# Kernel optimization log

Hardware: AMD Instinct MI355X
Metric: run time of the kernel (lower is better)

Reference implementation:

```python
import jax, jax.numpy as jnp
import numpy as np

# ---- static forest structure: 1024 complete binary trees of depth 9 ----
N_TREES = 1024
DEPTH = 9
NPT = 2 ** (DEPTH + 1) - 1            # 1023 nodes per tree
DIM = N_TREES * NPT                    # 1,047,552 total nodes
C = 10                                 # hidden states
M = 128                                # emission alphabet
N_GEN = 4                              # parallel generative models
LEVEL_SIZES = [N_TREES * 2 ** (k + 1) for k in range(DEPTH)]
LEVEL_START = np.concatenate([[0], np.cumsum(LEVEL_SIZES)]).astype(np.int64)
TREE_OFF = np.arange(N_TREES, dtype=np.int64) * NPT


def _build_forest():
    parents, children = [], []
    for k in range(DEPTH):
        ch = np.arange(2 ** (k + 1) - 1, 2 ** (k + 2) - 1, dtype=np.int64)  # depth k+1 nodes
        pa = (ch - 1) // 2                                                   # their parents (depth k)
        children.append((TREE_OFF[:, None] + ch[None, :]).ravel())
        parents.append((TREE_OFF[:, None] + pa[None, :]).ravel())
    leaves = (TREE_OFF[:, None] + np.arange(NPT // 2, NPT, dtype=np.int64)[None, :]).ravel()
    trees_ind = np.repeat(np.arange(N_TREES, dtype=np.int64), NPT)
    return np.concatenate(parents), np.concatenate(children), leaves, trees_ind


def setup_inputs() -> dict:
    key = jax.random.key(0)
    k1, k2, k3, k4 = jax.random.split(key, 4)
    parents, children, leaves, trees_ind = _build_forest()
    return {
        "x": jax.random.randint(k4, (DIM,), 0, M, dtype=jnp.int32),
        "A": jax.random.normal(k1, (C, C, N_GEN), jnp.float32) * 2.5,
        "B": jax.random.normal(k2, (C, M, N_GEN), jnp.float32) * 2.5,
        "Pi": jax.random.normal(k3, (C, N_GEN), jnp.float32) * 2.5,
        "parents": jnp.asarray(parents, jnp.int32),
        "children": jnp.asarray(children, jnp.int32),
        "trees_ind": jnp.asarray(trees_ind, jnp.int32),
        "leaves": jnp.asarray(leaves, jnp.int32),
    }


def _upward(x, A, B, Pi, parents, children, trees_ind, leaves):
    # softmax reparameterization (vectorized over the n_gen axis)
    smA = jax.nn.softmax(A, axis=0)    # P(parent state i | child state j), cols sum over i
    smB = jax.nn.softmax(B, axis=1)    # emission distribution per state
    smPi = jax.nn.softmax(Pi, axis=0)  # leaf prior

    beta = jnp.zeros((DIM, C, N_GEN), smA.dtype)
    t_beta = jnp.zeros((DIM, C, N_GEN), smA.dtype)
    ll = jnp.zeros((DIM, N_GEN), smA.dtype)

    # leaves: beta = Pi * B[:, x_leaf], normalized
    B_leaf = jnp.swapaxes(smB[:, x[leaves]], 0, 1)            # [L, C, G]
    b = smPi[None, :, :] * B_leaf
    nu = b.sum(axis=1)                                         # [L, G]
    beta = beta.at[leaves].set(b / nu[:, None, :])
    ll = ll.at[leaves].set(jnp.log(nu))

    # bottom-up sweep over levels (static loop over tree depth)
    for k in reversed(range(DEPTH)):
        s, e = int(LEVEL_START[k]), int(LEVEL_START[k + 1])
        pa, ch = parents[s:e], children[s:e]
        beta_ch = beta[ch]                                     # [E, C, G]
        tb_ch = jnp.einsum('ijg,ejg->eig', smA, beta_ch)       # sum over child state j
        sums = jax.ops.segment_sum(tb_ch, pa, num_segments=DIM)
        cnt = jax.ops.segment_sum(jnp.ones((e - s,), smA.dtype), pa, num_segments=DIM)
        t_beta = t_beta + sums / jnp.maximum(cnt, 1.0)[:, None, None]  # scatter-mean over children
        # unique parents at this level = all depth-k nodes (static for complete trees)
        u = jnp.asarray((TREE_OFF[:, None] + np.arange(2 ** k - 1, 2 ** (k + 1) - 1)[None, :]).ravel(), jnp.int32)
        B_u = jnp.swapaxes(smB[:, x[u]], 0, 1)                 # [U, C, G]
        bl = t_beta[u] * B_u
        nu = bl.sum(axis=1)
        beta = beta.at[u].set(bl / nu[:, None, :])
        ll = ll.at[u].set(jnp.log(nu))

    # per-tree log-likelihood: scatter-sum node terms over trees_ind
    return jax.ops.segment_sum(ll, trees_ind, num_segments=N_TREES)  # [n_trees, G]


def reference(x, A, B, Pi, parents, children, trees_ind, leaves):
    return _upward(x, A, B, Pi, parents, children, trees_ind, leaves)
```

## Files before the change

kernel.cpp:

```cpp
#include <hip/hip_runtime.h>
#include <math.h>

#define NC     10
#define NCP    12
#define NM     128
#define NGEN   4
#define NPT    1023
#define NTREES 1024

#define RCPF(x) __builtin_amdgcn_rcpf(x)
#define WAVE_FENCE() __builtin_amdgcn_wave_barrier()

struct F12 { float4 a, b, c; };

__device__ __forceinline__ F12 ld12(const float* p) {
    F12 r; const float4* q = (const float4*)p;
    r.a = q[0]; r.b = q[1]; r.c = q[2]; return r;
}
__device__ __forceinline__ void unpack10(float* t, const F12& r) {
    t[0] = r.a.x; t[1] = r.a.y; t[2] = r.a.z; t[3] = r.a.w;
    t[4] = r.b.x; t[5] = r.b.y; t[6] = r.b.z; t[7] = r.b.w;
    t[8] = r.c.x; t[9] = r.c.y;
}
__device__ __forceinline__ void fma10(float* t, const F12& c, float s) {
    t[0] += c.a.x * s; t[1] += c.a.y * s; t[2] += c.a.z * s; t[3] += c.a.w * s;
    t[4] += c.b.x * s; t[5] += c.b.y * s; t[6] += c.b.z * s; t[7] += c.b.w * s;
    t[8] += c.c.x * s; t[9] += c.c.y * s;
}
__device__ __forceinline__ void mul10(float* t, const F12& r) {
    t[0] *= r.a.x; t[1] *= r.a.y; t[2] *= r.a.z; t[3] *= r.a.w;
    t[4] *= r.b.x; t[5] *= r.b.y; t[6] *= r.b.z; t[7] *= r.b.w;
    t[8] *= r.c.x; t[9] *= r.c.y;
}
__device__ __forceinline__ float sum10(const float* v) {
    return (((v[0] + v[1]) + (v[2] + v[3])) + ((v[4] + v[5]) + (v[6] + v[7]))) + (v[8] + v[9]);
}

__device__ __forceinline__ float half_subtree(const F12* acol,
                                              const float (*sBT)[NCP],
                                              const float (*sBTpi)[NCP],
                                              int xl0, int xl1, int xl2, int xl3,
                                              int x8a, int x8b, int x7, float* b7out)
{
    float b0[NC], b1[NC], sc[NC], t8a[NC], t8b[NC];

    unpack10(b0, ld12(&sBTpi[xl0][0]));
    unpack10(b1, ld12(&sBTpi[xl1][0]));
    float nu0 = sum10(b0), nu1 = sum10(b1);
    #pragma unroll
    for (int j = 0; j < NC; ++j) sc[j] = b0[j] * nu1 + b1[j] * nu0;
    #pragma unroll
    for (int i = 0; i < NC; ++i) t8a[i] = 0.f;
    #pragma unroll
    for (int j = 0; j < NC; ++j) fma10(t8a, acol[j], sc[j]);
    mul10(t8a, ld12(&sBT[x8a][0]));
    const float nu8a = sum10(t8a);

    unpack10(b0, ld12(&sBTpi[xl2][0]));
    unpack10(b1, ld12(&sBTpi[xl3][0]));
    nu0 = sum10(b0); nu1 = sum10(b1);
    #pragma unroll
    for (int j = 0; j < NC; ++j) sc[j] = b0[j] * nu1 + b1[j] * nu0;
    #pragma unroll
    for (int i = 0; i < NC; ++i) t8b[i] = 0.f;
    #pragma unroll
    for (int j = 0; j < NC; ++j) fma10(t8b, acol[j], sc[j]);
    mul10(t8b, ld12(&sBT[x8b][0]));
    const float nu8b = sum10(t8b);

    #pragma unroll
    for (int j = 0; j < NC; ++j) sc[j] = t8a[j] * nu8b + t8b[j] * nu8a;
    float t7[NC];
    #pragma unroll
    for (int i = 0; i < NC; ++i) t7[i] = 0.f;
    #pragma unroll
    for (int j = 0; j < NC; ++j) fma10(t7, acol[j], sc[j]);
    mul10(t7, ld12(&sBT[x7][0]));
    const float nu7 = sum10(t7);
    const float r = RCPF(nu7);
    #pragma unroll
    for (int j = 0; j < NC; ++j) b7out[j] = t7[j] * r;
    return __logf(nu7);
}

__device__ __forceinline__ float fused_step_ip(const F12* acol, const float (*sBT)[NCP],
                                               float* buf, int l,
                                               int xc0, int xc1, int xp)
{
    float t0[NC], t1[NC];
    #pragma unroll
    for (int i = 0; i < NC; ++i) { t0[i] = 0.f; t1[i] = 0.f; }
    #pragma unroll
    for (int j = 0; j < NC; ++j) {
        float4 gv = *(const float4*)(buf + j * 64 + 4 * l);
        fma10(t0, acol[j], gv.x + gv.y);
        fma10(t1, acol[j], gv.z + gv.w);
    }
    mul10(t0, ld12(&sBT[xc0][0]));
    mul10(t1, ld12(&sBT[xc1][0]));
    const float nu0 = sum10(t0), nu1 = sum10(t1);
    float tp[NC];
    #pragma unroll
    for (int i = 0; i < NC; ++i) tp[i] = 0.f;
    #pragma unroll
    for (int j = 0; j < NC; ++j) fma10(tp, acol[j], t0[j] * nu1 + t1[j] * nu0);
    mul10(tp, ld12(&sBT[xp][0]));
    const float nup = sum10(tp);
    const float rp = RCPF(nup);
    #pragma unroll
    for (int j = 0; j < NC; ++j) buf[j * 64 + l] = tp[j] * rp;
    return __logf(nup);
}

__global__ __launch_bounds__(256, 2)
void htmm_fused(const int* __restrict__ x,
                const float* __restrict__ A,
                const float* __restrict__ B,
                const float* __restrict__ Pi,
                float* __restrict__ out)
{
    __shared__ __align__(16) float sACol[NC][NCP];
    __shared__ __align__(16) float sBT[NM][NCP];
    __shared__ __align__(16) float sBTpi[NM][NCP];
    __shared__ __align__(16) float sPiP[NCP];
    __shared__ __align__(16) float sB6[4][NC][64];

    const int bid = blockIdx.x;
    const int g = bid >> 8;
    const int treeBase = (bid & 255) * 4;
    const int tid = threadIdx.x;
    const int u = tid >> 6, lane = tid & 63;

    const int tree = treeBase + u;
    const int tb = tree * NPT;

    int xl[8];
    #pragma unroll
    for (int k = 0; k < 8; ++k) xl[k] = x[tb + 511 + 8 * lane + k];
    int x8v[4];
    #pragma unroll
    for (int c = 0; c < 4; ++c) x8v[c] = x[tb + 255 + 4 * lane + c];
    const int x7a = x[tb + 127 + 2 * lane];
    const int x7b = x[tb + 128 + 2 * lane];
    const int x6v = x[tb + 63 + lane];

    for (int c = u; c < NC; c += 4) {
        float e0 = __expf(B[(c * NM + lane) * NGEN + g]);
        float e1 = __expf(B[(c * NM + lane + 64) * NGEN + g]);
        float sm = e0 + e1;
        #pragma unroll
        for (int off = 32; off; off >>= 1) sm += __shfl_xor(sm, off);
        const float rs = 1.f / sm;
        sBT[lane][c]      = e0 * rs;
        sBT[lane + 64][c] = e1 * rs;
    }
    if (tid >= 128 && tid < 128 + NC) {
        const int j = tid - 128;
        float col[NC], mx = -1e30f;
        #pragma unroll
        for (int i = 0; i < NC; ++i) { col[i] = A[(i * NC + j) * NGEN + g]; mx = fmaxf(mx, col[i]); }
        float sm = 0.f;
        #pragma unroll
        for (int i = 0; i < NC; ++i) { col[i] = __expf(col[i] - mx); sm += col[i]; }
        const float rs = 0.5f / sm;
        #pragma unroll
        for (int i = 0; i < NC; ++i) sACol[j][i] = col[i] * rs;
    }
    if (tid == 192) {
        float col[NC], mx = -1e30f;
        #pragma unroll
        for (int i = 0; i < NC; ++i) { col[i] = Pi[i * NGEN + g]; mx = fmaxf(mx, col[i]); }
        float sm = 0.f;
        #pragma unroll
        for (int i = 0; i < NC; ++i) { col[i] = __expf(col[i] - mx); sm += col[i]; }
        const float rs = 1.f / sm;
        #pragma unroll
        for (int i = 0; i < NC; ++i) sPiP[i] = col[i] * rs;
    }
    __syncthreads();
    if (tid < NM) {
        F12 pi = ld12(sPiP);
        F12 r  = ld12(&sBT[tid][0]);
        sBTpi[tid][0] = pi.a.x * r.a.x; sBTpi[tid][1] = pi.a.y * r.a.y;
        sBTpi[tid][2] = pi.a.z * r.a.z; sBTpi[tid][3] = pi.a.w * r.a.w;
        sBTpi[tid][4] = pi.b.x * r.b.x; sBTpi[tid][5] = pi.b.y * r.b.y;
        sBTpi[tid][6] = pi.b.z * r.b.z; sBTpi[tid][7] = pi.b.w * r.b.w;
        sBTpi[tid][8] = pi.c.x * r.c.x; sBTpi[tid][9] = pi.c.y * r.c.y;
    }
    __syncthreads();

    F12 acol[NC];
    #pragma unroll
    for (int j = 0; j < NC; ++j) acol[j] = ld12(&sACol[j][0]);

    float b7a[NC], b7b[NC];
    float llacc;
    llacc  = half_subtree(acol, sBT, sBTpi, xl[0], xl[1], xl[2], xl[3],
                          x8v[0], x8v[1], x7a, b7a);
    llacc += half_subtree(acol, sBT, sBTpi, xl[4], xl[5], xl[6], xl[7],
                          x8v[2], x8v[3], x7b, b7b);

    {
        float sc[NC], t6[NC];
        #pragma unroll
        for (int j = 0; j < NC; ++j) sc[j] = b7a[j] + b7b[j];
        #pragma unroll
        for (int i = 0; i < NC; ++i) t6[i] = 0.f;
        #pragma unroll
        for (int j = 0; j < NC; ++j) fma10(t6, acol[j], sc[j]);
        mul10(t6, ld12(&sBT[x6v][0]));
        const float nup = sum10(t6);
        llacc += __logf(nup);
        const float rp = RCPF(nup);
        #pragma unroll
        for (int j = 0; j < NC; ++j) sB6[u][j][lane] = t6[j] * rp;
    }

    WAVE_FENCE();
    float lla = 0.f;
    if (lane < 16)
        lla = fused_step_ip(acol, sBT, &sB6[u][0][0], lane,
                            x[tb + 31 + 2 * lane], x[tb + 32 + 2 * lane],
                            x[tb + 15 + lane]);
    llacc += lla;
    WAVE_FENCE();
    float llb = 0.f;
    if (lane < 4)
        llb = fused_step_ip(acol, sBT, &sB6[u][0][0], lane,
                            x[tb + 7 + 2 * lane], x[tb + 8 + 2 * lane],
                            x[tb + 3 + lane]);
    llacc += llb;
    WAVE_FENCE();
    if (lane == 0)
        llacc += fused_step_ip(acol, sBT, &sB6[u][0][0], 0,
                               x[tb + 1], x[tb + 2], x[tb + 0]);

    #pragma unroll
    for (int off = 32; off; off >>= 1) llacc += __shfl_down(llacc, off);
    if (lane == 0) out[tree * NGEN + g] = llacc;
}

extern "C" void kernel_launch(void* const* d_in, const int* in_sizes, int n_in,
                              void* d_out, int out_size, void* d_ws, size_t ws_size,
                              hipStream_t stream) {
    const int*   x  = (const int*)d_in[0];
    const float* A  = (const float*)d_in[1];
    const float* B  = (const float*)d_in[2];
    const float* Pi = (const float*)d_in[3];
    float* out = (float*)d_out;
    htmm_fused<<<NTREES, 256, 0, stream>>>(x, A, B, Pi, out);
}
```

Before: 26.19 us.

## Consolidate top tree levels of four trees into one wavefront

After level 6, each wave reduces its partial log-likelihood to shared memory and the block synchronizes. Wave 0 then processes the top three levels for all four trees together, packing 16, 4 and 1 lanes per tree, while the other waves exit early. This removes three serial, mostly idle tail phases from three of the four waves. It adds a block-wide barrier and keeps the shared sB6 buffers live until wave 0 reads them.

```diff
diff --git a/kernel.cpp b/kernel.cpp
--- a/kernel.cpp
+++ b/kernel.cpp
@@ -124,6 +124,7 @@
     __shared__ __align__(16) float sBTpi[NM][NCP];
     __shared__ __align__(16) float sPiP[NCP];
     __shared__ __align__(16) float sB6[4][NC][64];
+    __shared__ float sll[4];
 
     const int bid = blockIdx.x;
     const int g = bid >> 8;
@@ -216,28 +217,44 @@
         for (int j = 0; j < NC; ++j) sB6[u][j][lane] = t6[j] * rp;
     }
 
+    #pragma unroll
+    for (int off = 32; off; off >>= 1) llacc += __shfl_down(llacc, off);
+    if (lane == 0) sll[u] = llacc;
+    __syncthreads();
+    if (u != 0) return;
+
+    {
+        const int tu = lane >> 4, l = lane & 15;
+        const int ttb = (treeBase + tu) * NPT;
+        float lla = fused_step_ip(acol, sBT, &sB6[tu][0][0], l,
+                                  x[ttb + 31 + 2 * l], x[ttb + 32 + 2 * l],
+                                  x[ttb + 15 + l]);
+        #pragma unroll
+        for (int off = 8; off; off >>= 1) lla += __shfl_down(lla, off, 16);
+        if (l == 0) sll[tu] += lla;
+    }
     WAVE_FENCE();
-    float lla = 0.f;
-    if (lane < 16)
-        lla = fused_step_ip(acol, sBT, &sB6[u][0][0], lane,
-                            x[tb + 31 + 2 * lane], x[tb + 32 + 2 * lane],
-                            x[tb + 15 + lane]);
-    llacc += lla;
+    if (lane < 16) {
+        const int tu = lane >> 2, l = lane & 3;
+        const int ttb = (treeBase + tu) * NPT;
+        float llb = fused_step_ip(acol, sBT, &sB6[tu][0][0], l,
+                                  x[ttb + 7 + 2 * l], x[ttb + 8 + 2 * l],
+                                  x[ttb + 3 + l]);
+        #pragma unroll
+        for (int off = 2; off; off >>= 1) llb += __shfl_down(llb, off, 4);
+        if (l == 0) sll[tu] += llb;
+    }
     WAVE_FENCE();
-    float llb = 0.f;
+    if (lane < 4) {
+        const int tu = lane;
+        const int ttb = (treeBase + tu) * NPT;
+        float llc = fused_step_ip(acol, sBT, &sB6[tu][0][0], 0,
+                                  x[ttb + 1], x[ttb + 2], x[ttb + 0]);
+        sll[tu] += llc;
+    }
+    WAVE_FENCE();
     if (lane < 4)
-        llb = fused_step_ip(acol, sBT, &sB6[u][0][0], lane,
-                            x[tb + 7 + 2 * lane], x[tb + 8 + 2 * lane],
-                            x[tb + 3 + lane]);
-    llacc += llb;
-    WAVE_FENCE();
-    if (lane == 0)
-        llacc += fused_step_ip(acol, sBT, &sB6[u][0][0], 0,
-                               x[tb + 1], x[tb + 2], x[tb + 0]);
-
-    #pragma unroll
-    for (int off = 32; off; off >>= 1) llacc += __shfl_down(llacc, off);
-    if (lane == 0) out[tree * NGEN + g] = llacc;
+        out[(treeBase + lane) * NGEN + g] = sll[lane];
 }
 
 extern "C" void kernel_launch(void* const* d_in, const int* in_sizes, int n_in,
```

Measured after the change: 24.89 us, median of 2. -5.0%, faster.
